# Optimization experiments

Hardware: AMD Instinct MI355X
Metric: run time of the kernel (lower is better)

The kernel has to match this reference:

```python
import jax, jax.numpy as jnp
import numpy as np

D_MIN, D_MAX, D_COUNT = 0.0, 20.0, 16  # RBF basis as in _rbf
EPS = 1e-6


def _rbf(d):
    # d: [...] -> [..., 16]
    mu = jnp.linspace(D_MIN, D_MAX, D_COUNT)
    sigma = (D_MAX - D_MIN) / D_COUNT
    return jnp.exp(-(((d[..., None] - mu) / sigma) ** 2))


def setup_inputs() -> dict:
    key = jax.random.key(0)
    k1, k2, k3 = jax.random.split(key, 3)
    N = 32768
    X = jax.random.normal(k1, (N, 4, 3), dtype=jnp.float32) * 10.0
    segment_ids = jax.random.randint(k2, (N,), 0, 3, dtype=jnp.int32)
    is_global = jax.random.randint(k3, (N,), 0, 2, dtype=jnp.int32).astype(bool)
    return {"X": X, "segment_ids": segment_ids, "is_global": is_global,
            "batch_size": 16, "top_k": 9}


def reference(X, segment_ids, is_global, batch_size, top_k):
    N = X.shape[0]
    B = batch_size
    L = N // B
    K = top_k

    # ---- per-batch dense pairwise distance + KNN (vectorized _knn_edges) ----
    Xca = X[:, 1, :].reshape(B, L, 3)                      # CA atoms per chain
    dX = Xca[:, :, None, :] - Xca[:, None, :, :]            # [B, L, L, 3]
    D = jnp.sqrt(jnp.sum(dX * dX, axis=-1) + EPS)           # [B, L, L]
    _, E_idx = jax.lax.top_k(-D, K)                         # smallest-K -> [B, L, K]

    offs = (jnp.arange(B, dtype=E_idx.dtype) * L)[:, None, None]
    col = (E_idx + offs).reshape(-1)                        # [N*K] global col idx
    row = jnp.repeat(jnp.arange(N, dtype=col.dtype), K)     # [N*K]

    row_seg, col_seg = segment_ids[row], segment_ids[col]
    not_global = jnp.logical_not(is_global[row] | is_global[col])
    ctx_mask = (row_seg == col_seg) & not_global            # ctx (intra-segment) edges
    inter_mask = (row_seg != col_seg) & not_global          # inter-segment edges

    # ---- node distance RBF features (get_node_dist) ----
    def node_d(i):
        return jnp.sqrt(jnp.sum((X[:, i, :] - X[:, 1, :]) ** 2, axis=1) + EPS)
    dis_node_feats = jnp.concatenate(
        [_rbf(node_d(0)), _rbf(node_d(2)), _rbf(node_d(3))], axis=1)  # [N, 48]

    # ---- edge distance RBF features on KNN edges (get_edge_dist) ----
    X_row, X_col = X[row], X[col]                           # [N*K, 4, 3]
    def edge_d(i):
        return jnp.sqrt(jnp.sum((X_row[:, i, :] - X_col[:, 1, :]) ** 2, axis=1) + EPS)
    dis_edge_feats = jnp.concatenate(
        [_rbf(edge_d(0)), _rbf(edge_d(1)), _rbf(edge_d(2)), _rbf(edge_d(3))],
        axis=1)                                             # [N*K, 64]

    return dis_node_feats, dis_edge_feats, row, col, ctx_mask, inter_mask
```

## Files before the change

kernel.cpp:

```cpp
#include <hip/hip_runtime.h>
#include <cstdint>
#include <cstddef>

#define NN   32768
#define BATCH 16
#define LL   2048
#define KNN  9
#define NE   (NN * KNN)
#define PLM  5
#define MTOP 12
#define RPW  4
#define TPB  1024
#define ROWS_PB ((TPB / 64) * RPW)


__device__ __forceinline__ float ref_d2(float ax, float ay, float az,
                                        float bx, float by, float bz) {
    float dx = __fsub_rn(ax, bx);
    float dy = __fsub_rn(ay, by);
    float dz = __fsub_rn(az, bz);
    return __fadd_rn(__fadd_rn(__fmul_rn(dx, dx), __fmul_rn(dy, dy)),
                     __fmul_rn(dz, dz));
}

__device__ __forceinline__ float ref_dist(float ax, float ay, float az,
                                          float bx, float by, float bz) {
    return sqrtf(__fadd_rn(ref_d2(ax, ay, az, bx, by, bz), 1e-6f));
}

__device__ __forceinline__ unsigned umed3(unsigned a, unsigned b, unsigned c) {
    unsigned r;
    asm("v_med3_u32 %0, %1, %2, %3" : "=v"(r) : "v"(a), "v"(b), "v"(c));
    return r;
}

__device__ __forceinline__ unsigned dpp_min16_ror(unsigned x) {
    unsigned t;
    t = (unsigned)__builtin_amdgcn_update_dpp(0, (int)x, 0x121, 0xf, 0xf, true);
    x = min(x, t);
    t = (unsigned)__builtin_amdgcn_update_dpp(0, (int)x, 0x122, 0xf, 0xf, true);
    x = min(x, t);
    t = (unsigned)__builtin_amdgcn_update_dpp(0, (int)x, 0x124, 0xf, 0xf, true);
    x = min(x, t);
    t = (unsigned)__builtin_amdgcn_update_dpp(0, (int)x, 0x128, 0xf, 0xf, true);
    x = min(x, t);
    return x;
}

__device__ __forceinline__ unsigned gather_min(unsigned a) {
    unsigned m0 = min((unsigned)__builtin_amdgcn_readlane((int)a, 15),
                      (unsigned)__builtin_amdgcn_readlane((int)a, 31));
    unsigned m1 = min((unsigned)__builtin_amdgcn_readlane((int)a, 47),
                      (unsigned)__builtin_amdgcn_readlane((int)a, 63));
    return min(m0, m1);
}

__global__ __launch_bounds__(TPB, 8) void fused_kernel(
    const float* __restrict__ X, const int* __restrict__ seg,
    const int* __restrict__ isg_raw,
    float* __restrict__ node_out, float* __restrict__ edge_out,
    float* __restrict__ out_row, float* __restrict__ out_col,
    float* __restrict__ out_ctx, float* __restrict__ out_inter)
{
    __shared__ float4 crd[LL];
    __shared__ float rowatoms[ROWS_PB * 12];
    __shared__ unsigned char code[LL];
    __shared__ int colsL[TPB / 64][RPW][KNN];
    __shared__ int flag;

    int tid  = threadIdx.x;
    int row0 = blockIdx.x * ROWS_PB;
    int base = row0 & ~(LL - 1);

    if (tid == 0) flag = 0;
    __syncthreads();
    if (tid < 512) {
        unsigned v = (unsigned)isg_raw[(base >> 2) + tid];
        if (v > 1u) atomicOr(&flag, 1);
    }
    if (tid < ROWS_PB * 12)
        rowatoms[tid] = X[(size_t)row0 * 12 + tid];
    __syncthreads();
    bool as_bytes = (flag != 0);
    for (int t = tid; t < LL; t += TPB) {
        const float* p = X + (size_t)(base + t) * 12 + 3;
        float x = p[0], y = p[1], z = p[2];
        crd[t] = make_float4(x, y, z, fmaf(x, x, fmaf(y, y, z * z)));
        int ig = as_bytes ? (int)((const unsigned char*)isg_raw)[base + t]
                          : isg_raw[base + t];
        code[t] = (unsigned char)((seg[base + t] & 3) | (ig ? 4 : 0));
    }
    __syncthreads();

    int lane = tid & 63;
    int warp = tid >> 6;
    int gi0  = row0 + warp * RPW;
    int i0   = gi0 - base;

    float qx2[RPW], qy2[RPW], qz2[RPW], qn1[RPW];
#pragma unroll
    for (int r = 0; r < RPW; ++r) {
        float4 ci = crd[i0 + r];
        qx2[r] = -2.0f * ci.x; qy2[r] = -2.0f * ci.y; qz2[r] = -2.0f * ci.z;
        qn1[r] = ci.w + 1.0f;
    }

    unsigned lst[RPW][PLM];
#pragma unroll
    for (int r = 0; r < RPW; ++r)
#pragma unroll
        for (int k = 0; k < PLM; ++k) lst[r][k] = 0xFFFFFFFFu;

#pragma unroll 8
    for (int s = 0; s < LL / 64; ++s) {
        int j = (s << 6) | lane;
        float4 c = crd[j];
#pragma unroll
        for (int r = 0; r < RPW; ++r) {
            float d2 = fmaf(qx2[r], c.x,
                       fmaf(qy2[r], c.y,
                       fmaf(qz2[r], c.z, qn1[r] + c.w)));
            unsigned cur = (__float_as_uint(d2) & 0xFFFFF800u) | (unsigned)j;
            unsigned n0 = min(lst[r][0], cur);
            unsigned n1 = umed3(lst[r][0], lst[r][1], cur);
            unsigned n2 = umed3(lst[r][1], lst[r][2], cur);
            unsigned n3 = umed3(lst[r][2], lst[r][3], cur);
            unsigned n4 = umed3(lst[r][3], lst[r][4], cur);
            lst[r][0] = n0; lst[r][1] = n1; lst[r][2] = n2;
            lst[r][3] = n3; lst[r][4] = n4;
        }
    }

    unsigned mine[RPW];
#pragma unroll
    for (int r = 0; r < RPW; ++r) mine[r] = 0xFFFFFFFFu;

#pragma unroll
    for (int t = 0; t < MTOP; ++t) {
        unsigned a[RPW], m[RPW];
#pragma unroll
        for (int r = 0; r < RPW; ++r) a[r] = dpp_min16_ror(lst[r][0]);
#pragma unroll
        for (int r = 0; r < RPW; ++r) m[r] = gather_min(a[r]);
#pragma unroll
        for (int r = 0; r < RPW; ++r) {
            bool rem = (lst[r][0] == m[r]);
#pragma unroll
            for (int k = 0; k < PLM - 1; ++k) lst[r][k] = rem ? lst[r][k + 1] : lst[r][k];
            lst[r][PLM - 1] = rem ? 0xFFFFFFFFu : lst[r][PLM - 1];
            mine[r] = (lane == t) ? m[r] : mine[r];
        }
    }

#pragma unroll
    for (int r = 0; r < RPW; ++r) {
        int gi = gi0 + r;
        int jf = (int)(mine[r] & (LL - 1));

        unsigned nbr = (unsigned)__builtin_amdgcn_update_dpp(
            (int)0xFFFFFFFF, (int)mine[r], 0x101 , 0xf, 0xf, false);
        bool tie = (lane < 11) && ((mine[r] ^ nbr) < 2048u);

        int rank;
        if (!__any(tie)) {
            rank = lane;
        } else {
            float4 ci = crd[i0 + r];
            float4 cj = crd[jf];
            float D = sqrtf(__fadd_rn(ref_d2(ci.x, ci.y, ci.z, cj.x, cj.y, cj.z), 1e-6f));
            rank = 0;
#pragma unroll
            for (int t = 0; t < MTOP; ++t) {
                float Dt = __int_as_float(__builtin_amdgcn_readlane(__float_as_int(D), t));
                int   jt = __builtin_amdgcn_readlane(jf, t);
                bool lt = (Dt < D) || (Dt == D && jt < jf);
                rank += lt ? 1 : 0;
            }
        }

        if (lane < MTOP && rank < KNN) {
            int cg = base + jf;
            int e  = gi * KNN + rank;
            out_row[e] = (float)gi;
            out_col[e] = (float)cg;
            int cr = code[gi - base], cc = code[jf];
            int ng = ((cr | cc) & 4) ? 0 : 1;
            int sr = cr & 3, sc = cc & 3;
            out_ctx[e]   = (sr == sc && ng) ? 1.0f : 0.0f;
            out_inter[e] = (sr != sc && ng) ? 1.0f : 0.0f;
            colsL[warp][r][rank] = jf;
        }
    }

    {
        int g = lane & 15, sE = lane >> 4;
        int atomE = g >> 2;
        float zk[4];
        float tbE = (float)((g & 3) * 4);
#pragma unroll
        for (int k = 0; k < 4; ++k)
            zk[k] = -(tbE + (float)k) * (20.0f / 15.0f) * 0.8f;
        int rA = warp * RPW;
        if (sE < 3) {
#pragma unroll
            for (int p = 0; p < 3 * RPW; ++p) {
                int r = p / 3;
                int q = (p % 3) * 3 + sE;
                int jf = colsL[warp][r][q];
                float4 cj = crd[jf];
                const float* ra = &rowatoms[(rA + r) * 12 + atomE * 3];
                float d = ref_dist(ra[0], ra[1], ra[2], cj.x, cj.y, cj.z);
                float4 v;
                float z0 = fmaf(d, 0.8f, zk[0]); v.x = __expf(-z0 * z0);
                float z1 = fmaf(d, 0.8f, zk[1]); v.y = __expf(-z1 * z1);
                float z2 = fmaf(d, 0.8f, zk[2]); v.z = __expf(-z2 * z2);
                float z3 = fmaf(d, 0.8f, zk[3]); v.w = __expf(-z3 * z3);
                *(float4*)(edge_out + ((size_t)(gi0 + r) * KNN + q) * 64 + g * 4) = v;
            }
        }
    }

    if (lane < 48) {
        int rn = lane / 12;
        int c4 = lane - rn * 12;
        int aN = c4 >> 2;
        int asrc = (aN == 0) ? 0 : aN + 1;
        float tbN = (float)((c4 & 3) * 4);
        float zn[4];
#pragma unroll
        for (int k = 0; k < 4; ++k)
            zn[k] = -(tbN + (float)k) * (20.0f / 15.0f) * 0.8f;
        const float* ra = &rowatoms[(warp * RPW + rn) * 12 + asrc * 3];
        float4 ca = crd[i0 + rn];
        float d = ref_dist(ra[0], ra[1], ra[2], ca.x, ca.y, ca.z);
        float4 v;
        float z0 = fmaf(d, 0.8f, zn[0]); v.x = __expf(-z0 * z0);
        float z1 = fmaf(d, 0.8f, zn[1]); v.y = __expf(-z1 * z1);
        float z2 = fmaf(d, 0.8f, zn[2]); v.z = __expf(-z2 * z2);
        float z3 = fmaf(d, 0.8f, zn[3]); v.w = __expf(-z3 * z3);
        *(float4*)(node_out + (size_t)(gi0 + rn) * 48 + c4 * 4) = v;
    }
}

extern "C" void kernel_launch(void* const* d_in, const int* in_sizes, int n_in,
                              void* d_out, int out_size, void* d_ws, size_t ws_size,
                              hipStream_t stream) {
    const float* X       = (const float*)d_in[0];
    const int*   seg     = (const int*)d_in[1];
    const int*   isg_raw = (const int*)d_in[2];

    float* out = (float*)d_out;
    float* node_out  = out;
    float* edge_out  = out + (size_t)NN * 48;
    float* row_out   = edge_out + (size_t)NE * 64;
    float* col_out   = row_out + NE;
    float* ctx_out   = col_out + NE;
    float* inter_out = ctx_out + NE;

    hipLaunchKernelGGL(fused_kernel, dim3(NN / ROWS_PB), dim3(TPB), 0, stream,
                       X, seg, isg_raw,
                       node_out, edge_out, row_out, col_out, ctx_out, inter_out);
}
```

Measured before the change: 48.99 us.

## Split shared coords into SoA and process four candidates per lane with packed FMA

Moves the shared-memory coordinate cache from float4 AoS to four separate x/y/z/norm arrays. Each lane now reads four consecutive candidates per step with float4 loads, computes their distances with 2-wide packed FMAs, and inserts all four into its sorted candidate list. The aim is fewer LDS instructions and packed FP32 math in the hot distance scan. The trade-off is that each lane now holds a different, strided subset of candidates, and later scalar lookups of single points need three separate LDS reads instead of one.

```diff
diff --git a/kernel.cpp b/kernel.cpp
--- a/kernel.cpp
+++ b/kernel.cpp
@@ -13,6 +13,8 @@
 #define TPB  1024
 #define ROWS_PB ((TPB / 64) * RPW)
 
+typedef float vf2 __attribute__((ext_vector_type(2)));
+
 
 __device__ __forceinline__ float ref_d2(float ax, float ay, float az,
                                         float bx, float by, float bz) {
@@ -34,6 +36,15 @@
     return r;
 }
 
+__device__ __forceinline__ void insert5(unsigned* l, unsigned cur) {
+    unsigned n0 = min(l[0], cur);
+    unsigned n1 = umed3(l[0], l[1], cur);
+    unsigned n2 = umed3(l[1], l[2], cur);
+    unsigned n3 = umed3(l[2], l[3], cur);
+    unsigned n4 = umed3(l[3], l[4], cur);
+    l[0] = n0; l[1] = n1; l[2] = n2; l[3] = n3; l[4] = n4;
+}
+
 __device__ __forceinline__ unsigned dpp_min16_ror(unsigned x) {
     unsigned t;
     t = (unsigned)__builtin_amdgcn_update_dpp(0, (int)x, 0x121, 0xf, 0xf, true);
@@ -62,7 +73,7 @@
     float* __restrict__ out_row, float* __restrict__ out_col,
     float* __restrict__ out_ctx, float* __restrict__ out_inter)
 {
-    __shared__ float4 crd[LL];
+    __shared__ float sx[LL], sy[LL], sz[LL], sn[LL];
     __shared__ float rowatoms[ROWS_PB * 12];
     __shared__ unsigned char code[LL];
     __shared__ int colsL[TPB / 64][RPW][KNN];
@@ -85,7 +96,8 @@
     for (int t = tid; t < LL; t += TPB) {
         const float* p = X + (size_t)(base + t) * 12 + 3;
         float x = p[0], y = p[1], z = p[2];
-        crd[t] = make_float4(x, y, z, fmaf(x, x, fmaf(y, y, z * z)));
+        sx[t] = x; sy[t] = y; sz[t] = z;
+        sn[t] = fmaf(x, x, fmaf(y, y, z * z));
         int ig = as_bytes ? (int)((const unsigned char*)isg_raw)[base + t]
                           : isg_raw[base + t];
         code[t] = (unsigned char)((seg[base + t] & 3) | (ig ? 4 : 0));
@@ -100,9 +112,10 @@
     float qx2[RPW], qy2[RPW], qz2[RPW], qn1[RPW];
 #pragma unroll
     for (int r = 0; r < RPW; ++r) {
-        float4 ci = crd[i0 + r];
-        qx2[r] = -2.0f * ci.x; qy2[r] = -2.0f * ci.y; qz2[r] = -2.0f * ci.z;
-        qn1[r] = ci.w + 1.0f;
+        qx2[r] = -2.0f * sx[i0 + r];
+        qy2[r] = -2.0f * sy[i0 + r];
+        qz2[r] = -2.0f * sz[i0 + r];
+        qn1[r] = sn[i0 + r] + 1.0f;
     }
 
     unsigned lst[RPW][PLM];
@@ -112,22 +125,36 @@
         for (int k = 0; k < PLM; ++k) lst[r][k] = 0xFFFFFFFFu;
 
 #pragma unroll 8
-    for (int s = 0; s < LL / 64; ++s) {
-        int j = (s << 6) | lane;
-        float4 c = crd[j];
+    for (int s = 0; s < LL / 256; ++s) {
+        int j = (s << 8) | (lane << 2);
+        float4 cx = *(const float4*)&sx[j];
+        float4 cy = *(const float4*)&sy[j];
+        float4 cz = *(const float4*)&sz[j];
+        float4 cn = *(const float4*)&sn[j];
+        vf2 cx01 = {cx.x, cx.y}, cx23 = {cx.z, cx.w};
+        vf2 cy01 = {cy.x, cy.y}, cy23 = {cy.z, cy.w};
+        vf2 cz01 = {cz.x, cz.y}, cz23 = {cz.z, cz.w};
+        vf2 cn01 = {cn.x, cn.y}, cn23 = {cn.z, cn.w};
 #pragma unroll
         for (int r = 0; r < RPW; ++r) {
-            float d2 = fmaf(qx2[r], c.x,
-                       fmaf(qy2[r], c.y,
-                       fmaf(qz2[r], c.z, qn1[r] + c.w)));
-            unsigned cur = (__float_as_uint(d2) & 0xFFFFF800u) | (unsigned)j;
-            unsigned n0 = min(lst[r][0], cur);
-            unsigned n1 = umed3(lst[r][0], lst[r][1], cur);
-            unsigned n2 = umed3(lst[r][1], lst[r][2], cur);
-            unsigned n3 = umed3(lst[r][2], lst[r][3], cur);
-            unsigned n4 = umed3(lst[r][3], lst[r][4], cur);
-            lst[r][0] = n0; lst[r][1] = n1; lst[r][2] = n2;
-            lst[r][3] = n3; lst[r][4] = n4;
+            vf2 qx = {qx2[r], qx2[r]};
+            vf2 qy = {qy2[r], qy2[r]};
+            vf2 qz = {qz2[r], qz2[r]};
+            vf2 qn = {qn1[r], qn1[r]};
+            vf2 d01 = __builtin_elementwise_fma(qx, cx01,
+                      __builtin_elementwise_fma(qy, cy01,
+                      __builtin_elementwise_fma(qz, cz01, qn + cn01)));
+            vf2 d23 = __builtin_elementwise_fma(qx, cx23,
+                      __builtin_elementwise_fma(qy, cy23,
+                      __builtin_elementwise_fma(qz, cz23, qn + cn23)));
+            unsigned c0 = (__float_as_uint(d01.x) & 0xFFFFF800u) | (unsigned)(j + 0);
+            unsigned c1 = (__float_as_uint(d01.y) & 0xFFFFF800u) | (unsigned)(j + 1);
+            unsigned c2 = (__float_as_uint(d23.x) & 0xFFFFF800u) | (unsigned)(j + 2);
+            unsigned c3 = (__float_as_uint(d23.y) & 0xFFFFF800u) | (unsigned)(j + 3);
+            insert5(lst[r], c0);
+            insert5(lst[r], c1);
+            insert5(lst[r], c2);
+            insert5(lst[r], c3);
         }
     }
 
@@ -165,9 +192,9 @@
         if (!__any(tie)) {
             rank = lane;
         } else {
-            float4 ci = crd[i0 + r];
-            float4 cj = crd[jf];
-            float D = sqrtf(__fadd_rn(ref_d2(ci.x, ci.y, ci.z, cj.x, cj.y, cj.z), 1e-6f));
+            float qxr = sx[i0 + r], qyr = sy[i0 + r], qzr = sz[i0 + r];
+            float cjx = sx[jf], cjy = sy[jf], cjz = sz[jf];
+            float D = sqrtf(__fadd_rn(ref_d2(qxr, qyr, qzr, cjx, cjy, cjz), 1e-6f));
             rank = 0;
 #pragma unroll
             for (int t = 0; t < MTOP; ++t) {
@@ -207,9 +234,9 @@
                 int r = p / 3;
                 int q = (p % 3) * 3 + sE;
                 int jf = colsL[warp][r][q];
-                float4 cj = crd[jf];
+                float cjx = sx[jf], cjy = sy[jf], cjz = sz[jf];
                 const float* ra = &rowatoms[(rA + r) * 12 + atomE * 3];
-                float d = ref_dist(ra[0], ra[1], ra[2], cj.x, cj.y, cj.z);
+                float d = ref_dist(ra[0], ra[1], ra[2], cjx, cjy, cjz);
                 float4 v;
                 float z0 = fmaf(d, 0.8f, zk[0]); v.x = __expf(-z0 * z0);
                 float z1 = fmaf(d, 0.8f, zk[1]); v.y = __expf(-z1 * z1);
@@ -231,8 +258,8 @@
         for (int k = 0; k < 4; ++k)
             zn[k] = -(tbN + (float)k) * (20.0f / 15.0f) * 0.8f;
         const float* ra = &rowatoms[(warp * RPW + rn) * 12 + asrc * 3];
-        float4 ca = crd[i0 + rn];
-        float d = ref_dist(ra[0], ra[1], ra[2], ca.x, ca.y, ca.z);
+        float cax = sx[i0 + rn], cay = sy[i0 + rn], caz = sz[i0 + rn];
+        float d = ref_dist(ra[0], ra[1], ra[2], cax, cay, caz);
         float4 v;
         float z0 = fmaf(d, 0.8f, zn[0]); v.x = __expf(-z0 * z0);
         float z1 = fmaf(d, 0.8f, zn[1]); v.y = __expf(-z1 * z1);
```

New measurement: 51.73 us. +5.6%, slower.
